# Kernel optimization log

Measured on AMD Instinct MI355X. Metric: run time of the kernel, lower is better.

## Reference

```python
import jax, jax.numpy as jnp
import numpy as np

DIM = 768
HEADS = 12
WS = 8       # window_size
EPS = 1e-5   # torch LayerNorm eps


def _ln(x, g, b):
    m = jnp.mean(x, axis=-1, keepdims=True)
    v = jnp.var(x, axis=-1, keepdims=True)
    return (x - m) / jnp.sqrt(v + EPS) * g + b


def _attention(xw, qkv_w, proj_w, proj_b):
    # xw: (Bw, N, C) with N = WS*WS
    Bw, N, C = xw.shape
    D = C // HEADS
    scale = D ** -0.5
    # torch does x.reshape(3, B, N, C//3): a flat row-major split, identical in jax
    x3 = xw.reshape(3, Bw, N, C // 3)
    def tile(t):  # cat((t,t,t)) then reshape(B,N,C), exactly as torch
        return jnp.concatenate([t, t, t], axis=0).reshape(Bw, N, C)
    red, green, blue = tile(x3[0]), tile(x3[1]), tile(x3[2])
    # qkv Linear has no bias (qkv_bias=False); only k,v of Red and q of Green/Blue
    # are used, and q_green + q_blue == (green+blue) @ Wq^T
    Wq, Wk, Wv = qkv_w[:C], qkv_w[C:2 * C], qkv_w[2 * C:]
    def heads(t):  # (Bw,N,C) -> (Bw,H,N,D)
        return t.reshape(Bw, N, HEADS, D).transpose(0, 2, 1, 3)
    q = heads((green + blue) @ Wq.T)
    k = heads(red @ Wk.T)
    v = heads(red @ Wv.T)
    attn = jax.nn.softmax(jnp.einsum('bhnd,bhmd->bhnm', q, k) * scale, axis=-1)
    out = jnp.einsum('bhnm,bhmd->bhnd', attn, v).transpose(0, 2, 1, 3).reshape(Bw, N, C)
    return out @ proj_w.T + proj_b


def setup_inputs() -> dict:
    key = jax.random.key(0)
    ks = jax.random.split(key, 6)
    B, H, W, C = 4, 128, 128, DIM
    def p(k, shape):
        return jax.random.normal(k, shape, jnp.float32) * 0.02
    return {
        'x': jax.random.normal(ks[0], (B, H * W, C), jnp.float32),
        'norm1_g': jnp.ones((C,), jnp.float32),
        'norm1_b': jnp.zeros((C,), jnp.float32),
        'norm2_g': jnp.ones((C,), jnp.float32),
        'norm2_b': jnp.zeros((C,), jnp.float32),
        'qkv_w': p(ks[1], (3 * C, C)),
        'proj_w': p(ks[2], (C, C)),
        'proj_b': jnp.zeros((C,), jnp.float32),
        'fc1_w': p(ks[3], (1, C)),   # Mlp hidden_features hardcoded to 1 in source
        'fc1_b': jnp.zeros((1,), jnp.float32),
        'fc2_w': p(ks[4], (C, 1)),
        'fc2_b': jnp.zeros((C,), jnp.float32),
        'h': 128,
        'w': 128,
    }


def reference(x, norm1_g, norm1_b, norm2_g, norm2_b, qkv_w, proj_w, proj_b,
              fc1_w, fc1_b, fc2_w, fc2_b, h, w):
    B, L, C = x.shape
    xn = _ln(x, norm1_g, norm1_b).reshape(B, h, w, C)
    # window_partition: (B,H,W,C) -> (nW*B, WS*WS, C)
    xw = xn.reshape(B, h // WS, WS, w // WS, WS, C)
    xw = xw.transpose(0, 1, 3, 2, 4, 5).reshape(-1, WS * WS, C)
    a = _attention(xw, qkv_w, proj_w, proj_b)
    a = _ln(a, norm2_g, norm2_b)
    # NOTE: source has NO residual connections; output is mlp(norm2(attn(...)))
    hdn = jax.nn.gelu(a @ fc1_w.T + fc1_b, approximate=False)  # torch GELU = exact erf
    m = hdn @ fc2_w.T + fc2_b
    return m.reshape(B, h * w, C)
```

## Files before the change

kernel.cpp:

```cpp
#include <hip/hip_runtime.h>
#include <hip/hip_bf16.h>
#include <stdint.h>
#include <stddef.h>

typedef __bf16 bf16;
typedef __bf16 bf16x4 __attribute__((ext_vector_type(4)));
typedef __bf16 bf16x8 __attribute__((ext_vector_type(8)));
typedef float  f32x4  __attribute__((ext_vector_type(4)));

__device__ __forceinline__ void async16(const void* src, void* dst) {
    __builtin_amdgcn_global_load_lds(
        (__attribute__((address_space(1))) void*)(void*)(src),
        (__attribute__((address_space(3))) void*)(dst),
        16, 0, 0);
}

#define MEMFENCE asm volatile("" ::: "memory")

__global__ __launch_bounds__(256)
void f2b(const float* __restrict__ src, bf16* __restrict__ dst, int n)
{
    const int i = (blockIdx.x * 256 + threadIdx.x) * 4;
    if (i < n) {
        f32x4 c = *(const f32x4*)(src + i);
        bf16x4 o;
        #pragma unroll
        for (int q = 0; q < 4; ++q) o[q] = (bf16)c[q];
        *(bf16x4*)(dst + i) = o;
    }
}

__global__ __launch_bounds__(256)
void ln1_win(const float* __restrict__ x, const float* __restrict__ g,
             const float* __restrict__ b, bf16* __restrict__ Y)
{
    const int row  = blockIdx.x * 4 + (threadIdx.x >> 6);
    const int lane = threadIdx.x & 63;
    const float* xr = x + (size_t)row * 768;
    float v[12];
    float sum = 0.f, ssq = 0.f;
    #pragma unroll
    for (int j = 0; j < 3; ++j) {
        f32x4 c = *(const f32x4*)(xr + j * 256 + lane * 4);
        #pragma unroll
        for (int q = 0; q < 4; ++q) {
            float f = c[q];
            v[j * 4 + q] = f; sum += f; ssq += f * f;
        }
    }
    #pragma unroll
    for (int d = 1; d < 64; d <<= 1) {
        sum += __shfl_xor(sum, d, 64);
        ssq += __shfl_xor(ssq, d, 64);
    }
    const float mean = sum * (1.f / 768.f);
    const float rstd = rsqrtf(ssq * (1.f / 768.f) - mean * mean + 1e-5f);
    const int bb = row >> 14;
    const int l  = row & 16383;
    const int hy = l >> 7, wx = l & 127;
    const int m  = ((bb * 256 + (hy >> 3) * 16 + (wx >> 3)) << 6)
                 + ((hy & 7) << 3) + (wx & 7);
    bf16* yr = Y + (size_t)m * 768;
    #pragma unroll
    for (int j = 0; j < 3; ++j) {
        const int c0 = j * 256 + lane * 4;
        f32x4 gg = *(const f32x4*)(g + c0);
        f32x4 bv = *(const f32x4*)(b + c0);
        bf16x4 ov;
        #pragma unroll
        for (int q = 0; q < 4; ++q)
            ov[q] = (bf16)((v[j * 4 + q] - mean) * rstd * gg[q] + bv[q]);
        *(bf16x4*)(yr + c0) = ov;
    }
}

__global__ __launch_bounds__(256)
void gsum(const bf16* __restrict__ Y, bf16* __restrict__ G, int Smod)
{
    const int i = (blockIdx.x * 256 + threadIdx.x) * 8;
    if (i < Smod) {
        bf16x8 a = *(const bf16x8*)(Y + Smod + i);
        bf16x8 c = *(const bf16x8*)(Y + 2 * Smod + i);
        bf16x8 r;
        #pragma unroll
        for (int q = 0; q < 8; ++q) r[q] = (bf16)((float)a[q] + (float)c[q]);
        *(bf16x8*)(G + i) = r;
    }
}

template<int AMODE, bool BIAS, bool NT>
__global__ __launch_bounds__(512, 2)
void gemm_bt(const bf16* __restrict__ A, const bf16* __restrict__ Yg,
             const bf16* __restrict__ Gb, const bf16* __restrict__ Bm,
             const float* __restrict__ bias, bf16* __restrict__ Cm,
             int K, int ldc, int Smod, int nb_n)
{
    constexpr int ABUF = 128 * 64;
    constexpr int BBUF = 256 * 64;
    constexpr int BUF  = ABUF + BBUF;
    __shared__ bf16 lds[3 * BUF];

    const int per    = gridDim.x >> 3;
    const int mchunk = per / nb_n;
    const int xcd    = blockIdx.x & 7;
    const int slot_b = blockIdx.x >> 3;
    const int mbase  = (xcd * mchunk + slot_b / nb_n) * 128;
    const int nbase  = (slot_b % nb_n) * 256;

    const int tid  = threadIdx.x;
    const int lane = tid & 63;
    const int w    = tid >> 6;
    const int quad = lane >> 4;
    const int l16  = lane & 15;
    const int wm   = (w >> 2) * 64;
    const int wn   = (w & 3) * 64;
    const int rsub = lane >> 3;
    const int slot = lane & 7;

    const bf16* Asrc = (AMODE == 1) ? ((nbase < 768) ? Gb : Yg) : A;
    const int nt = K >> 6;

    auto stageA = [&](int t, int kt, bf16* Ab) {
        const int row = 16 * w + 8 * t + rsub;
        const int kc  = slot ^ (row & 7);
        const bf16* s;
        if (AMODE == 1) {
            int f = (mbase + row) * 768 + kt * 64 + kc * 8;
            if (f >= 2 * Smod) f -= 2 * Smod;
            else if (f >= Smod) f -= Smod;
            s = Asrc + f;
        } else {
            s = Asrc + (size_t)(mbase + row) * K + kt * 64 + kc * 8;
        }
        async16(s, Ab + (16 * w + 8 * t) * 64);
    };
    auto stageB = [&](int t, int kt, bf16* Bb) {
        const int row = 32 * w + 8 * t + rsub;
        const int kc  = slot ^ (row & 7);
        async16(Bm + (size_t)(nbase + row) * K + kt * 64 + kc * 8,
                Bb + (32 * w + 8 * t) * 64);
    };

    const f32x4 zero = {0.f, 0.f, 0.f, 0.f};
    f32x4 acc[4][4];
    #pragma unroll
    for (int i = 0; i < 4; ++i)
        #pragma unroll
        for (int j = 0; j < 4; ++j) acc[i][j] = zero;

    auto compute = [&](int ks, const bf16* Ab, const bf16* Bb) {
        bf16x8 af[4], bfr[4];
        #pragma unroll
        for (int i = 0; i < 4; ++i) {
            const int row = wm + 16 * i + l16;
            const int sl  = (ks * 4 + quad) ^ (row & 7);
            af[i] = *(const bf16x8*)(Ab + row * 64 + sl * 8);
        }
        #pragma unroll
        for (int j = 0; j < 4; ++j) {
            const int row = wn + 16 * j + l16;
            const int sl  = (ks * 4 + quad) ^ (row & 7);
            bfr[j] = *(const bf16x8*)(Bb + row * 64 + sl * 8);
        }
        __builtin_amdgcn_s_setprio(1);
        #pragma unroll
        for (int i = 0; i < 4; ++i)
            #pragma unroll
            for (int j = 0; j < 4; ++j)
                acc[i][j] = __builtin_amdgcn_mfma_f32_16x16x32_bf16(
                    af[i], bfr[j], acc[i][j], 0, 0, 0);
        __builtin_amdgcn_s_setprio(0);
    };

    {
        bf16* Ab = lds;        bf16* Bb = lds + ABUF;
        stageA(0, 0, Ab); stageA(1, 0, Ab);
        stageB(0, 0, Bb); stageB(1, 0, Bb); stageB(2, 0, Bb); stageB(3, 0, Bb);
        if (nt > 1) {
            bf16* A1 = lds + BUF; bf16* B1 = lds + BUF + ABUF;
            stageA(0, 1, A1); stageA(1, 1, A1);
            stageB(0, 1, B1); stageB(1, 1, B1); stageB(2, 1, B1); stageB(3, 1, B1);
            asm volatile("s_waitcnt vmcnt(6)" ::: "memory");
        } else {
            asm volatile("s_waitcnt vmcnt(0)" ::: "memory");
        }
    }
    __builtin_amdgcn_s_barrier();
    MEMFENCE;

    int cur = 0;
    for (int t = 0; t < nt; ++t) {
        bf16* Ab = lds + cur * BUF;
        bf16* Bb = Ab + ABUF;
        const int nx = (cur + 2 >= 3) ? cur - 1 : cur + 2;
        bf16* An = lds + nx * BUF;
        bf16* Bn = An + ABUF;
        const bool pf = (t + 2 < nt);

        if (pf) { stageA(0, t + 2, An); stageB(0, t + 2, Bn); stageB(1, t + 2, Bn); }
        compute(0, Ab, Bb);
        __builtin_amdgcn_s_barrier();
        MEMFENCE;

        if (pf) { stageA(1, t + 2, An); stageB(2, t + 2, Bn); stageB(3, t + 2, Bn); }
        compute(1, Ab, Bb);
        if (t < nt - 2) { asm volatile("s_waitcnt vmcnt(6)" ::: "memory"); }
        else            { asm volatile("s_waitcnt vmcnt(0)" ::: "memory"); }
        __builtin_amdgcn_s_barrier();
        MEMFENCE;

        cur = (cur + 1 == 3) ? 0 : cur + 1;
    }

    #pragma unroll
    for (int i = 0; i < 4; ++i) {
        const int row0 = mbase + wm + 16 * i + quad * 4;
        #pragma unroll
        for (int j = 0; j < 4; ++j) {
            const int col = nbase + wn + 16 * j + l16;
            float bv = 0.f;
            if (BIAS) bv = bias[col];
            #pragma unroll
            for (int r = 0; r < 4; ++r) {
                bf16 val = (bf16)(acc[i][j][r] + bv);
                bf16* p = Cm + (size_t)(row0 + r) * ldc + col;
                if (NT) {
                    unsigned short u = __builtin_bit_cast(unsigned short, val);
                    __builtin_nontemporal_store(u, (unsigned short*)p);
                } else {
                    *p = val;
                }
            }
        }
    }
}

__global__ __launch_bounds__(64)
void attn_win(const bf16* __restrict__ QKV, bf16* __restrict__ AOut)
{
    const int blk  = blockIdx.x;
    const int bw   = blk / 12;
    const int h    = blk % 12;
    const int lane = threadIdx.x;
    const int quad = lane >> 4;
    const int l16  = lane & 15;

    __shared__ bf16 Kt[64 * 64];
    __shared__ bf16 Vt[64 * 64];

    const size_t rowbase = (size_t)bw * 64;

    {
        const int rsub = lane >> 3;
        const int slot = lane & 7;
        #pragma unroll
        for (int t = 0; t < 8; ++t) {
            const int row = 8 * t + rsub;
            const int kcK = slot ^ (row & 7);
            async16(QKV + (rowbase + row) * 2304 + 768 + h * 64 + kcK * 8,
                    Kt + (8 * t) * 64);
            async16(QKV + (rowbase + row) * 2304 + 1536 + h * 64 + slot * 8,
                    Vt + (8 * t) * 64);
        }
    }

    bf16x8 qf[4][2];
    #pragma unroll
    for (int i = 0; i < 4; ++i)
        #pragma unroll
        for (int ks = 0; ks < 2; ++ks)
            qf[i][ks] = *(const bf16x8*)(QKV + (rowbase + 16 * i + l16) * 2304
                                         + h * 64 + ks * 32 + quad * 8);
    __syncthreads();

    const f32x4 zero = {0.f, 0.f, 0.f, 0.f};
    f32x4 s[4][4];
    #pragma unroll
    for (int i = 0; i < 4; ++i)
        #pragma unroll
        for (int j = 0; j < 4; ++j) s[i][j] = zero;

    #pragma unroll
    for (int ks = 0; ks < 2; ++ks) {
        bf16x8 kf[4];
        #pragma unroll
        for (int j = 0; j < 4; ++j) {
            const int row  = 16 * j + l16;
            const int slot = (ks * 4 + quad) ^ (row & 7);
            kf[j] = *(const bf16x8*)(Kt + row * 64 + slot * 8);
        }
        #pragma unroll
        for (int i = 0; i < 4; ++i)
            #pragma unroll
            for (int j = 0; j < 4; ++j)
                s[i][j] = __builtin_amdgcn_mfma_f32_16x16x32_bf16(
                    qf[i][ks], kf[j], s[i][j], 0, 0, 0);
    }

    float rrec[4][4];
    #pragma unroll
    for (int i = 0; i < 4; ++i) {
        #pragma unroll
        for (int r = 0; r < 4; ++r) {
            float mx = s[i][0][r];
            #pragma unroll
            for (int j = 1; j < 4; ++j) mx = fmaxf(mx, s[i][j][r]);
            #pragma unroll
            for (int d = 1; d < 16; d <<= 1) mx = fmaxf(mx, __shfl_xor(mx, d, 64));
            float sum = 0.f;
            #pragma unroll
            for (int j = 0; j < 4; ++j) {
                float p = __expf((s[i][j][r] - mx) * 0.125f);
                s[i][j][r] = p;
                sum += p;
            }
            #pragma unroll
            for (int d = 1; d < 16; d <<= 1) sum += __shfl_xor(sum, d, 64);
            rrec[i][r] = 1.f / sum;
        }
    }

    #pragma unroll
    for (int i = 0; i < 4; ++i)
        #pragma unroll
        for (int j = 0; j < 4; ++j)
            #pragma unroll
            for (int r = 0; r < 4; ++r) {
                const int row  = 16 * i + quad * 4 + r;
                const int col  = 16 * j + l16;
                const int slot = (col >> 3) ^ (row & 7);
                Kt[row * 64 + slot * 8 + (col & 7)] = (bf16)s[i][j][r];
            }
    __syncthreads();

    f32x4 o[4][4];
    #pragma unroll
    for (int i = 0; i < 4; ++i)
        #pragma unroll
        for (int j = 0; j < 4; ++j) o[i][j] = zero;

    #pragma unroll
    for (int ks = 0; ks < 2; ++ks) {
        bf16x8 pf[4], vf[4];
        #pragma unroll
        for (int i = 0; i < 4; ++i) {
            const int row  = 16 * i + l16;
            const int slot = (ks * 4 + quad) ^ (row & 7);
            pf[i] = *(const bf16x8*)(Kt + row * 64 + slot * 8);
        }
        #pragma unroll
        for (int j = 0; j < 4; ++j) {
            bf16x8 t;
            #pragma unroll
            for (int q = 0; q < 8; ++q)
                t[q] = Vt[(ks * 32 + quad * 8 + q) * 64 + 16 * j + l16];
            vf[j] = t;
        }
        #pragma unroll
        for (int i = 0; i < 4; ++i)
            #pragma unroll
            for (int j = 0; j < 4; ++j)
                o[i][j] = __builtin_amdgcn_mfma_f32_16x16x32_bf16(
                    pf[i], vf[j], o[i][j], 0, 0, 0);
    }

    #pragma unroll
    for (int i = 0; i < 4; ++i)
        #pragma unroll
        for (int j = 0; j < 4; ++j)
            #pragma unroll
            for (int r = 0; r < 4; ++r) {
                const size_t grow = rowbase + 16 * i + quad * 4 + r;
                const int col = h * 64 + 16 * j + l16;
                AOut[grow * 768 + col] = (bf16)(o[i][j][r] * rrec[i][r]);
            }
}

__global__ __launch_bounds__(256)
void final_fused(const bf16* __restrict__ P, const float* __restrict__ g2,
                 const float* __restrict__ b2, const float* __restrict__ fc1w,
                 const float* __restrict__ fc1b, const float* __restrict__ fc2w,
                 const float* __restrict__ fc2b, float* __restrict__ out)
{
    const int row  = blockIdx.x * 4 + (threadIdx.x >> 6);
    const int lane = threadIdx.x & 63;
    const bf16* pr = P + (size_t)row * 768;
    float v[12];
    float sum = 0.f, ssq = 0.f;
    #pragma unroll
    for (int j = 0; j < 3; ++j) {
        bf16x4 c = *(const bf16x4*)(pr + j * 256 + lane * 4);
        #pragma unroll
        for (int q = 0; q < 4; ++q) {
            float f = (float)c[q];
            v[j * 4 + q] = f; sum += f; ssq += f * f;
        }
    }
    #pragma unroll
    for (int d = 1; d < 64; d <<= 1) {
        sum += __shfl_xor(sum, d, 64);
        ssq += __shfl_xor(ssq, d, 64);
    }
    const float mean = sum * (1.f / 768.f);
    const float rstd = rsqrtf(ssq * (1.f / 768.f) - mean * mean + 1e-5f);
    float part = 0.f;
    #pragma unroll
    for (int j = 0; j < 3; ++j) {
        const int c0 = j * 256 + lane * 4;
        f32x4 gg = *(const f32x4*)(g2 + c0);
        f32x4 bb = *(const f32x4*)(b2 + c0);
        f32x4 f1 = *(const f32x4*)(fc1w + c0);
        #pragma unroll
        for (int q = 0; q < 4; ++q) {
            float ln = (v[j * 4 + q] - mean) * rstd * gg[q] + bb[q];
            part += ln * f1[q];
        }
    }
    #pragma unroll
    for (int d = 1; d < 64; d <<= 1) part += __shfl_xor(part, d, 64);
    const float sv = part + fc1b[0];
    const float ge = 0.5f * sv * (1.f + erff(sv * 0.70710678118654752f));
    float* orow = out + (size_t)row * 768;
    #pragma unroll
    for (int j = 0; j < 3; ++j) {
        const int c0 = j * 256 + lane * 4;
        f32x4 f2  = *(const f32x4*)(fc2w + c0);
        f32x4 b2v = *(const f32x4*)(fc2b + c0);
        f32x4 ov;
        #pragma unroll
        for (int q = 0; q < 4; ++q)
            ov[q] = ge * f2[q] + b2v[q];
        *(f32x4*)(orow + c0) = ov;
    }
}

extern "C" void kernel_launch(void* const* d_in, const int* in_sizes, int n_in,
                              void* d_out, int out_size, void* d_ws, size_t ws_size,
                              hipStream_t stream)
{
    const float* x     = (const float*)d_in[0];
    const float* n1g   = (const float*)d_in[1];
    const float* n1b   = (const float*)d_in[2];
    const float* n2g   = (const float*)d_in[3];
    const float* n2b   = (const float*)d_in[4];
    const float* qkvw  = (const float*)d_in[5];
    const float* projw = (const float*)d_in[6];
    const float* projb = (const float*)d_in[7];
    const float* fc1w  = (const float*)d_in[8];
    const float* fc1b  = (const float*)d_in[9];
    const float* fc2w  = (const float*)d_in[10];
    const float* fc2b  = (const float*)d_in[11];
    float* out = (float*)d_out;

    const int total = in_sizes[0];
    const int rows  = total / 768;
    const int Smod  = total / 3;
    const int Bw    = rows / 64;
    const int C     = 768;

    bf16* qkv     = (bf16*)d_ws;
    bf16* Ybuf    = qkv + (size_t)rows * 2304;
    bf16* qkvw_b  = Ybuf + (size_t)rows * 768;
    bf16* projw_b = qkvw_b + (size_t)3 * C * C;
    bf16* Pbuf    = qkv;
    bf16* Gb      = (bf16*)d_out;

    const int nqkvw  = 3 * C * C;
    const int nprojw = C * C;
    f2b<<<(nqkvw / 4 + 255) / 256, 256, 0, stream>>>(qkvw, qkvw_b, nqkvw);
    f2b<<<(nprojw / 4 + 255) / 256, 256, 0, stream>>>(projw, projw_b, nprojw);

    ln1_win<<<rows / 4, 256, 0, stream>>>(x, n1g, n1b, Ybuf);

    gsum<<<(Smod / 8 + 255) / 256, 256, 0, stream>>>(Ybuf, Gb, Smod);

    const int nbm = rows / 128;
    gemm_bt<1, false, true><<<nbm * 9, 512, 0, stream>>>(
        nullptr, Ybuf, Gb, qkvw_b, nullptr, qkv, 768, 2304, Smod, 9);

    attn_win<<<Bw * 12, 64, 0, stream>>>(qkv, Ybuf);

    gemm_bt<0, true, false><<<nbm * 3, 512, 0, stream>>>(
        Ybuf, nullptr, nullptr, projw_b, projb, Pbuf, 768, 768, 0, 3);

    final_fused<<<rows / 4, 256, 0, stream>>>(Pbuf, n2g, n2b, fc1w, fc1b,
                                              fc2w, fc2b, out);
}
```

Before: 909.0 us.

## Enlarge GEMM tile to 256x256 with 8-phase double-buffered pipeline

Replaces the 128x256 triple-buffered GEMM with a 256x256 tile where each wave computes a 128x64 sub-tile, using two LDS buffers split into half-K slices. The main loop runs in eight phases that interleave LDS reads, async global-to-LDS staging and MFMA bursts, separated by barriers. This raises arithmetic intensity per block and is meant to cut global and LDS traffic per FLOP. The costs are twice the accumulator registers (which may limit occupancy under launch bounds 512,2), more barriers per K step, and half as many blocks. The nontemporal store option for the QKV output is dropped.

```diff
diff --git a/kernel.cpp b/kernel.cpp
--- a/kernel.cpp
+++ b/kernel.cpp
@@ -16,6 +16,12 @@
 }
 
 #define MEMFENCE asm volatile("" ::: "memory")
+
+__device__ __forceinline__ void barrier_f() {
+    MEMFENCE;
+    __builtin_amdgcn_s_barrier();
+    MEMFENCE;
+}
 
 __global__ __launch_bounds__(256)
 void f2b(const float* __restrict__ src, bf16* __restrict__ dst, int n)
@@ -88,23 +94,20 @@
     }
 }
 
-template<int AMODE, bool BIAS, bool NT>
+template<int AMODE, bool BIAS>
 __global__ __launch_bounds__(512, 2)
-void gemm_bt(const bf16* __restrict__ A, const bf16* __restrict__ Yg,
-             const bf16* __restrict__ Gb, const bf16* __restrict__ Bm,
-             const float* __restrict__ bias, bf16* __restrict__ Cm,
-             int K, int ldc, int Smod, int nb_n)
-{
-    constexpr int ABUF = 128 * 64;
-    constexpr int BBUF = 256 * 64;
-    constexpr int BUF  = ABUF + BBUF;
-    __shared__ bf16 lds[3 * BUF];
+void gemm8p(const bf16* __restrict__ A, const bf16* __restrict__ Yg,
+            const bf16* __restrict__ Gb, const bf16* __restrict__ Bm,
+            const float* __restrict__ bias, bf16* __restrict__ Cm,
+            int K, int ldc, int Smod, int nb_n)
+{
+    __shared__ bf16 lds[2 * 32768];
 
     const int per    = gridDim.x >> 3;
     const int mchunk = per / nb_n;
     const int xcd    = blockIdx.x & 7;
     const int slot_b = blockIdx.x >> 3;
-    const int mbase  = (xcd * mchunk + slot_b / nb_n) * 128;
+    const int mbase  = (xcd * mchunk + slot_b / nb_n) * 256;
     const int nbase  = (slot_b % nb_n) * 256;
 
     const int tid  = threadIdx.x;
@@ -112,108 +115,118 @@
     const int w    = tid >> 6;
     const int quad = lane >> 4;
     const int l16  = lane & 15;
-    const int wm   = (w >> 2) * 64;
+    const int wm   = (w >> 2) * 128;
     const int wn   = (w & 3) * 64;
-    const int rsub = lane >> 3;
-    const int slot = lane & 7;
 
     const bf16* Asrc = (AMODE == 1) ? ((nbase < 768) ? Gb : Yg) : A;
     const int nt = K >> 6;
 
-    auto stageA = [&](int t, int kt, bf16* Ab) {
-        const int row = 16 * w + 8 * t + rsub;
-        const int kc  = slot ^ (row & 7);
-        const bf16* s;
-        if (AMODE == 1) {
-            int f = (mbase + row) * 768 + kt * 64 + kc * 8;
-            if (f >= 2 * Smod) f -= 2 * Smod;
-            else if (f >= Smod) f -= Smod;
-            s = Asrc + f;
-        } else {
-            s = Asrc + (size_t)(mbase + row) * K + kt * 64 + kc * 8;
-        }
-        async16(s, Ab + (16 * w + 8 * t) * 64);
+    auto stage = [&](int kt, int X, int ks) {
+        bf16* base = lds + (kt & 1) * 32768 + X * 16384 + ks * 8192;
+        const int kb = kt * 64 + ks * 32;
+        #pragma unroll
+        for (int c = 0; c < 2; ++c) {
+            const int idx = tid + c * 512;
+            const int r   = idx >> 2;
+            const int q   = (idx & 3) ^ ((r >> 1) & 3);
+            const bf16* s;
+            if (X == 0) {
+                if (AMODE == 1) {
+                    int f = (mbase + r) * 768 + kb + q * 8;
+                    if (f >= 2 * Smod) f -= 2 * Smod;
+                    else if (f >= Smod) f -= Smod;
+                    s = Asrc + f;
+                } else {
+                    s = Asrc + (size_t)(mbase + r) * K + kb + q * 8;
+                }
+            } else {
+                s = Bm + (size_t)(nbase + r) * K + kb + q * 8;
+            }
+            async16(s, base + idx * 8);
+        }
     };
-    auto stageB = [&](int t, int kt, bf16* Bb) {
-        const int row = 32 * w + 8 * t + rsub;
-        const int kc  = slot ^ (row & 7);
-        async16(Bm + (size_t)(nbase + row) * K + kt * 64 + kc * 8,
-                Bb + (32 * w + 8 * t) * 64);
+
+    auto readA = [&](bf16x8* af, int kt, int ks) {
+        const bf16* base = lds + (kt & 1) * 32768 + ks * 8192;
+        #pragma unroll
+        for (int i = 0; i < 8; ++i) {
+            const int r = wm + 16 * i + l16;
+            const int q = quad ^ ((r >> 1) & 3);
+            af[i] = *(const bf16x8*)(base + r * 32 + q * 8);
+        }
     };
+    auto readB = [&](bf16x8* bfr, int kt, int ks, int nh) {
+        const bf16* base = lds + (kt & 1) * 32768 + 16384 + ks * 8192;
+        #pragma unroll
+        for (int j = 0; j < 2; ++j) {
+            const int r = wn + nh * 32 + 16 * j + l16;
+            const int q = quad ^ ((r >> 1) & 3);
+            bfr[j] = *(const bf16x8*)(base + r * 32 + q * 8);
+        }
+    };
 
     const f32x4 zero = {0.f, 0.f, 0.f, 0.f};
-    f32x4 acc[4][4];
-    #pragma unroll
-    for (int i = 0; i < 4; ++i)
+    f32x4 acc[8][4];
+    #pragma unroll
+    for (int i = 0; i < 8; ++i)
         #pragma unroll
         for (int j = 0; j < 4; ++j) acc[i][j] = zero;
 
-    auto compute = [&](int ks, const bf16* Ab, const bf16* Bb) {
-        bf16x8 af[4], bfr[4];
-        #pragma unroll
-        for (int i = 0; i < 4; ++i) {
-            const int row = wm + 16 * i + l16;
-            const int sl  = (ks * 4 + quad) ^ (row & 7);
-            af[i] = *(const bf16x8*)(Ab + row * 64 + sl * 8);
-        }
-        #pragma unroll
-        for (int j = 0; j < 4; ++j) {
-            const int row = wn + 16 * j + l16;
-            const int sl  = (ks * 4 + quad) ^ (row & 7);
-            bfr[j] = *(const bf16x8*)(Bb + row * 64 + sl * 8);
-        }
+    auto mma16 = [&](const bf16x8* af, const bf16x8* bfr, int nh) {
         __builtin_amdgcn_s_setprio(1);
         #pragma unroll
-        for (int i = 0; i < 4; ++i)
-            #pragma unroll
-            for (int j = 0; j < 4; ++j)
-                acc[i][j] = __builtin_amdgcn_mfma_f32_16x16x32_bf16(
-                    af[i], bfr[j], acc[i][j], 0, 0, 0);
+        for (int i = 0; i < 8; ++i)
+            #pragma unroll
+            for (int jj = 0; jj < 2; ++jj)
+                acc[i][nh * 2 + jj] = __builtin_amdgcn_mfma_f32_16x16x32_bf16(
+                    af[i], bfr[jj], acc[i][nh * 2 + jj], 0, 0, 0);
         __builtin_amdgcn_s_setprio(0);
     };
 
-    {
-        bf16* Ab = lds;        bf16* Bb = lds + ABUF;
-        stageA(0, 0, Ab); stageA(1, 0, Ab);
-        stageB(0, 0, Bb); stageB(1, 0, Bb); stageB(2, 0, Bb); stageB(3, 0, Bb);
-        if (nt > 1) {
-            bf16* A1 = lds + BUF; bf16* B1 = lds + BUF + ABUF;
-            stageA(0, 1, A1); stageA(1, 1, A1);
-            stageB(0, 1, B1); stageB(1, 1, B1); stageB(2, 1, B1); stageB(3, 1, B1);
-            asm volatile("s_waitcnt vmcnt(6)" ::: "memory");
-        } else {
-            asm volatile("s_waitcnt vmcnt(0)" ::: "memory");
-        }
-    }
-    __builtin_amdgcn_s_barrier();
-    MEMFENCE;
-
-    int cur = 0;
-    for (int t = 0; t < nt; ++t) {
-        bf16* Ab = lds + cur * BUF;
-        bf16* Bb = Ab + ABUF;
-        const int nx = (cur + 2 >= 3) ? cur - 1 : cur + 2;
-        bf16* An = lds + nx * BUF;
-        bf16* Bn = An + ABUF;
-        const bool pf = (t + 2 < nt);
-
-        if (pf) { stageA(0, t + 2, An); stageB(0, t + 2, Bn); stageB(1, t + 2, Bn); }
-        compute(0, Ab, Bb);
-        __builtin_amdgcn_s_barrier();
-        MEMFENCE;
-
-        if (pf) { stageA(1, t + 2, An); stageB(2, t + 2, Bn); stageB(3, t + 2, Bn); }
-        compute(1, Ab, Bb);
-        if (t < nt - 2) { asm volatile("s_waitcnt vmcnt(6)" ::: "memory"); }
-        else            { asm volatile("s_waitcnt vmcnt(0)" ::: "memory"); }
-        __builtin_amdgcn_s_barrier();
-        MEMFENCE;
-
-        cur = (cur + 1 == 3) ? 0 : cur + 1;
-    }
-
-    #pragma unroll
-    for (int i = 0; i < 4; ++i) {
+    stage(0, 0, 0); stage(0, 1, 0); stage(0, 0, 1); stage(0, 1, 1);
+    if (nt > 1) { stage(1, 0, 0); stage(1, 1, 0); }
+    asm volatile("s_waitcnt vmcnt(8)" ::: "memory");
+    barrier_f();
+
+    bf16x8 af[8], bfr[2];
+    for (int kt = 0; kt < nt; ++kt) {
+        readA(af, kt, 0);
+        readB(bfr, kt, 0, 0);
+        if (kt + 1 < nt) stage(kt + 1, 0, 1);
+        barrier_f();
+        asm volatile("s_waitcnt lgkmcnt(0)" ::: "memory");
+        mma16(af, bfr, 0);
+        barrier_f();
+
+        readB(bfr, kt, 0, 1);
+        if (kt + 1 < nt) stage(kt + 1, 1, 1);
+        if (kt < nt - 2) asm volatile("s_waitcnt vmcnt(6)" ::: "memory");
+        else             asm volatile("s_waitcnt vmcnt(0)" ::: "memory");
+        barrier_f();
+        asm volatile("s_waitcnt lgkmcnt(0)" ::: "memory");
+        mma16(af, bfr, 1);
+        barrier_f();
+
+        readA(af, kt, 1);
+        readB(bfr, kt, 1, 0);
+        if (kt + 2 < nt) stage(kt + 2, 0, 0);
+        barrier_f();
+        asm volatile("s_waitcnt lgkmcnt(0)" ::: "memory");
+        mma16(af, bfr, 0);
+        barrier_f();
+
+        readB(bfr, kt, 1, 1);
+        if (kt + 2 < nt) stage(kt + 2, 1, 0);
+        if (kt < nt - 2) asm volatile("s_waitcnt vmcnt(6)" ::: "memory");
+        else             asm volatile("s_waitcnt vmcnt(0)" ::: "memory");
+        barrier_f();
+        asm volatile("s_waitcnt lgkmcnt(0)" ::: "memory");
+        mma16(af, bfr, 1);
+        barrier_f();
+    }
+
+    #pragma unroll
+    for (int i = 0; i < 8; ++i) {
         const int row0 = mbase + wm + 16 * i + quad * 4;
         #pragma unroll
         for (int j = 0; j < 4; ++j) {
@@ -221,16 +234,8 @@
             float bv = 0.f;
             if (BIAS) bv = bias[col];
             #pragma unroll
-            for (int r = 0; r < 4; ++r) {
-                bf16 val = (bf16)(acc[i][j][r] + bv);
-                bf16* p = Cm + (size_t)(row0 + r) * ldc + col;
-                if (NT) {
-                    unsigned short u = __builtin_bit_cast(unsigned short, val);
-                    __builtin_nontemporal_store(u, (unsigned short*)p);
-                } else {
-                    *p = val;
-                }
-            }
+            for (int r = 0; r < 4; ++r)
+                Cm[(size_t)(row0 + r) * ldc + col] = (bf16)(acc[i][j][r] + bv);
         }
     }
 }
@@ -474,13 +479,13 @@
 
     gsum<<<(Smod / 8 + 255) / 256, 256, 0, stream>>>(Ybuf, Gb, Smod);
 
-    const int nbm = rows / 128;
-    gemm_bt<1, false, true><<<nbm * 9, 512, 0, stream>>>(
+    const int nbm = rows / 256;
+    gemm8p<1, false><<<nbm * 9, 512, 0, stream>>>(
         nullptr, Ybuf, Gb, qkvw_b, nullptr, qkv, 768, 2304, Smod, 9);
 
     attn_win<<<Bw * 12, 64, 0, stream>>>(qkv, Ybuf);
 
-    gemm_bt<0, true, false><<<nbm * 3, 512, 0, stream>>>(
+    gemm8p<0, true><<<nbm * 3, 512, 0, stream>>>(
         Ybuf, nullptr, nullptr, projw_b, projb, Pbuf, 768, 768, 0, 3);
 
     final_fused<<<rows / 4, 256, 0, stream>>>(Pbuf, n2g, n2b, fc1w, fc1b,
```

Measured after the change: 867.6 us. 1.05x faster.
